# Kernel tuning notes

Measured on AMD Instinct MI355X. Metric: run time of the kernel, lower is better.

## Reference

```python
import jax, jax.numpy as jnp
import numpy as np
from jax import lax

N_SECTIONS, N_CHANNELS = 8, 128
KT, KF = 32, 16                 # kernel (time, freq)
LPOST = 400                     # section_length_postsyn
LPRE = KT + LPOST - 1           # 431, section_length_presyn
SECTION_DISTANCE = 400          # LPRE - overlap (overlap = 31)
N_TIMESTEPS, FREQ = 3231, 256
THRESHOLD = 15.0


def setup_inputs() -> dict:
    key = jax.random.key(0)
    k1, k2 = jax.random.split(key)
    # scale so mean conv response ~ threshold (512 taps * 0.8 * mean(X))
    X = jax.random.uniform(k1, (N_TIMESTEPS, FREQ), dtype=jnp.float32) * 0.073
    # SpykeTorch Convolution init: N(0.8, 0.05)
    W = 0.8 + 0.05 * jax.random.normal(k2, (N_SECTIONS, N_CHANNELS, 1, KT, KF), dtype=jnp.float32)
    return {"X": X, "W": W}


def _sections(X):
    # [S, LPRE, FREQ] overlapping time windows
    starts = jnp.arange(N_SECTIONS) * SECTION_DISTANCE
    idx = starts[:, None] + jnp.arange(LPRE)
    return X[idx]


def _conv_sections(X, W):
    Xs = _sections(X)  # [S, LPRE, FREQ]
    def conv1(xs, w):
        # xs: [LPRE, FREQ], w: [C, 1, KT, KF] -> [C, LPOST, FOUT]
        return lax.conv_general_dilated(xs[None, None], w, (1, 1), 'VALID')[0]
    return jax.vmap(conv1)(Xs, W)  # [S, C, LPOST, FOUT]


def reference(X, W):
    pots = _conv_sections(X, W)                              # [S, C, 400, 241]
    # sf.fire: zero potentials < threshold, then sign -> binary spikes
    spikes = (pots >= THRESHOLD).astype(pots.dtype)
    # Pooling((LPOST, KF)): max-pool, stride = window, no padding
    pool = lax.reduce_window(spikes, -jnp.inf, lax.max,
                             (1, 1, LPOST, KF), (1, 1, LPOST, KF), 'VALID')  # [S, C, 1, 15]
    # sf.get_k_winners(pool): dim 0 (sections) acts as the time dimension
    T = pool.shape[0]
    spk = jnp.sign(pool)
    earliest = jnp.clip((T - spk.sum(axis=0)).astype(jnp.int32), 0, T - 1)   # [C,1,Fp]
    values = jnp.take_along_axis(pool, earliest[None], axis=0)[0]            # earliest spike value
    trunc = spk * values[None]
    v = trunc.max() * T
    trunc = trunc + spk * v
    total = trunc.sum(axis=0)                                # [C, 1, Fp]
    max_val = total.max()
    # winners[0][0] = feature (channel) index of the flat argmax
    feat = jnp.argmax(total.reshape(-1)) // (total.shape[1] * total.shape[2])
    return jnp.where(max_val != 0, feat, -1).astype(jnp.int32)
```

## Files before the change

### kernel.cpp

```cpp
#include <hip/hip_runtime.h>


using int2v  = __attribute__((ext_vector_type(2))) int;
using int4v  = __attribute__((ext_vector_type(4))) int;
using int8v  = __attribute__((ext_vector_type(8))) int;
using f32x8  = __attribute__((ext_vector_type(8))) float;
using f32x16 = __attribute__((ext_vector_type(16))) float;

#define SCALE_ONE 0x7F7F7F7F
#define THRESH_Q  4920.0f

#if __has_builtin(__builtin_amdgcn_cvt_scalef32_pk_fp4_f32)
#define HWFP4 1
#else
#define HWFP4 0
#endif

__device__ __forceinline__ unsigned f4enc(float v) {
  float r2 = __builtin_rintf(v + v);
  float r1 = __builtin_rintf(v);
  return (v <= 2.f) ? (unsigned)r2
       : (v <= 4.f) ? (unsigned)r1 + 2u
       : (v < 5.f)  ? 6u : 7u;
}

__device__ __forceinline__ unsigned pack8(f32x8 v) {
  unsigned d = 0;
#if HWFP4
  d = __builtin_amdgcn_cvt_scalef32_pk_fp4_f32(d, v[0], v[1], 1.0f, 0);
  d = __builtin_amdgcn_cvt_scalef32_pk_fp4_f32(d, v[2], v[3], 1.0f, 1);
  d = __builtin_amdgcn_cvt_scalef32_pk_fp4_f32(d, v[4], v[5], 1.0f, 2);
  d = __builtin_amdgcn_cvt_scalef32_pk_fp4_f32(d, v[6], v[7], 1.0f, 3);
#else
#pragma unroll
  for (int e = 0; e < 8; ++e) d |= f4enc(v[e]) << (4 * e);
#endif
  return d;
}

__global__ __launch_bounds__(256) void prep_kernel(const float* __restrict__ W,
                                                   unsigned char* __restrict__ Wp4,
                                                   int* __restrict__ pool) {
  int t = blockIdx.x * 256 + threadIdx.x;
  if (t < 15360) pool[t] = 0;
  int s = t >> 11, r = t & 2047, c = r >> 4, b = r & 15;
  const float* src = W + ((s * 128 + c) * 512 + b * 32);
  int4v o;
#pragma unroll
  for (int i = 0; i < 4; ++i) {
    f32x8 sv;
#pragma unroll
    for (int e = 0; e < 8; ++e) sv[e] = fmaxf(src[i * 8 + e], 0.f) * 4.f;
    o[i] = (int)pack8(sv);
  }
  *(int4v*)(Wp4 + s * 32768 + (b >> 1) * 4096 + (b & 1) * 2048 + c * 16) = o;
}

__global__ __launch_bounds__(512, 2) void conv_pool_kernel(const float* __restrict__ X,
                                                           const unsigned char* __restrict__ Wp4,
                                                           int* __restrict__ pool) {
  __shared__ __align__(16) unsigned char Ash[2][8 * 512];
  __shared__ unsigned poolbits[2][32];

  const int tid = threadIdx.x;
  const int s   = blockIdx.x & 7;
  const int lb  = blockIdx.x >> 3;
  const int NT  = (lb < 6) ? 13 : 12;

  const int ok  = tid < 504;
  const int it0 = ok ? tid : 0;
  const int d0  = it0 / 63, r0 = it0 % 63;
  const float* Xs = X + (s * 400 + r0) * 256 + d0;

  const int w = tid >> 6, l = tid & 63;
  const int m31 = l & 31, ko = l >> 5;
  const int aoff = w * 512 + m31 * 8 + ko * 16;

  if (tid < 64) poolbits[tid >> 5][tid & 31] = 0;

  f32x8 xa, xb;
  {
    int tau = lb, tt = tau / 30, ft = tau % 30;
    int t0 = (tt == 12) ? 368 : tt * 32;
    const float* xp = Xs + t0 * 256 + ft * 8;
#pragma unroll
    for (int e = 0; e < 8; ++e) { xa[e] = xp[e]; xb[e] = xp[e + 8]; }
  }
  __builtin_amdgcn_sched_barrier(0);

  int4v Breg[8][4];
  {
    const unsigned char* wb = Wp4 + s * 32768 + ko * 2048 + m31 * 16;
#pragma unroll
    for (int ch = 0; ch < 8; ++ch)
#pragma unroll
      for (int nt = 0; nt < 4; ++nt)
        Breg[ch][nt] = *(const int4v*)(wb + ch * 4096 + nt * 512);
  }

  xa *= 82.f; xb *= 82.f;
  if (ok) *(int2v*)&Ash[0][d0 * 512 + r0 * 8] = (int2v){(int)pack8(xa), (int)pack8(xb)};
  if (NT > 1) {
    int tau = lb + 32, tt = tau / 30, ft = tau % 30;
    int t0 = (tt == 12) ? 368 : tt * 32;
    const float* xp = Xs + t0 * 256 + ft * 8;
#pragma unroll
    for (int e = 0; e < 8; ++e) { xa[e] = xp[e]; xb[e] = xp[e + 8]; }
  }
  __syncthreads();

#pragma unroll 1
  for (int i = 0; i < NT; ++i) {
    const unsigned char* ab = &Ash[i & 1][0];

    f32x16 acc[4];
#pragma unroll
    for (int b = 0; b < 4; ++b)
#pragma unroll
      for (int e = 0; e < 16; ++e) acc[b][e] = 0.f;
#pragma unroll
    for (int ch = 0; ch < 8; ++ch) {
      int2v alo = *(const int2v*)&ab[aoff + ch * 32];
      int2v ahi = *(const int2v*)&ab[aoff + ch * 32 + 8];
      int8v Af = {alo[0], alo[1], ahi[0], ahi[1], 0, 0, 0, 0};
#pragma unroll
      for (int nt = 0; nt < 4; ++nt) {
        int8v Bf = {Breg[ch][nt][0], Breg[ch][nt][1],
                    Breg[ch][nt][2], Breg[ch][nt][3], 0, 0, 0, 0};
        acc[nt] = __builtin_amdgcn_mfma_scale_f32_32x32x64_f8f6f4(
            Af, Bf, acc[nt], 4, 4, 0, SCALE_ONE, 0, SCALE_ONE);
      }
    }

    unsigned sp = 0;
#pragma unroll
    for (int nt = 0; nt < 4; ++nt) {
      float m0 = -1e30f;
#pragma unroll
      for (int e = 0; e < 16; ++e) m0 = fmaxf(m0, acc[nt][e]);
      if (m0 >= THRESH_Q) sp |= (1u << nt);
    }
    sp |= __shfl_xor(sp, 32, 64);
    if (l < 32 && sp) atomicOr(&poolbits[i & 1][m31], sp);

    if (i + 1 < NT) {
      xa *= 82.f; xb *= 82.f;
      if (ok)
        *(int2v*)&Ash[(i + 1) & 1][d0 * 512 + r0 * 8] =
            (int2v){(int)pack8(xa), (int)pack8(xb)};
      if (i + 2 < NT) {
        int tau = lb + 32 * (i + 2), tt = tau / 30, ft = tau % 30;
        int t0 = (tt == 12) ? 368 : tt * 32;
        const float* xp = Xs + t0 * 256 + ft * 8;
#pragma unroll
        for (int e = 0; e < 8; ++e) { xa[e] = xp[e]; xb[e] = xp[e + 8]; }
      }
    }

    __syncthreads();

    if (tid < 32) {
      unsigned bits = poolbits[i & 1][tid];
      poolbits[i & 1][tid] = 0;
      if (bits) {
        int tau = lb + 32 * i;
        int fp = (tau % 30) >> 1;
#pragma unroll
        for (int nt = 0; nt < 4; ++nt)
          if ((bits >> nt) & 1)
            pool[(s * 128 + nt * 32 + tid) * 15 + fp] = 1;
      }
    }
  }
}

__global__ __launch_bounds__(256) void winner_kernel(const int* __restrict__ pool,
                                                     float* __restrict__ out) {
  __shared__ int lp[15360];
  __shared__ int sh_v;
  __shared__ int sh_best;
  int tid = threadIdx.x;
  if (tid == 0) { sh_v = 0; sh_best = 0; }
  for (int i = tid; i < 15360; i += 256) lp[i] = pool[i];
  __syncthreads();

  int localv = 0;
  for (int p = tid; p < 1920; p += 256) {
    int c = p / 15, f = p % 15;
    int cnt = 0;
    for (int s = 0; s < 8; ++s) cnt += lp[(s * 128 + c) * 15 + f];
    if (cnt > 0) {
      int early = 8 - cnt; if (early > 7) early = 7;
      localv |= lp[(early * 128 + c) * 15 + f];
    }
  }
  if (localv) atomicOr(&sh_v, 1);
  __syncthreads();

  const int v = sh_v * 8;
  int localbest = 0;
  for (int p = tid; p < 1920; p += 256) {
    int c = p / 15, f = p % 15;
    int cnt = 0;
    for (int s = 0; s < 8; ++s) cnt += lp[(s * 128 + c) * 15 + f];
    int early = 8 - cnt; if (early > 7) early = 7;
    int val = lp[(early * 128 + c) * 15 + f];
    int total = cnt * (val + v);
    int pack = (total << 12) | (4095 - p);
    if (pack > localbest) localbest = pack;
  }
  atomicMax(&sh_best, localbest);
  __syncthreads();

  if (tid == 0) {
    int total = sh_best >> 12;
    int p = 4095 - (sh_best & 4095);
    int feat = p / 15;
    out[0] = (total != 0) ? (float)feat : -1.0f;
  }
}

extern "C" void kernel_launch(void* const* d_in, const int* in_sizes, int n_in,
                              void* d_out, int out_size, void* d_ws, size_t ws_size,
                              hipStream_t stream) {
  (void)in_sizes; (void)n_in; (void)out_size; (void)ws_size;
  const float* X = (const float*)d_in[0];
  const float* W = (const float*)d_in[1];
  unsigned char* Wp4 = (unsigned char*)d_ws;
  int* pool = (int*)((char*)d_ws + (1 << 18));

  prep_kernel<<<64, 256, 0, stream>>>(W, Wp4, pool);
  conv_pool_kernel<<<256, 512, 0, stream>>>(X, Wp4, pool);
  winner_kernel<<<1, 256, 0, stream>>>(pool, (float*)d_out);
}
```

Baseline: 86.99 us.

## Fuse winner selection into conv kernel via last-block pattern and bitmask pool

Replaces the per-element int pool array with a 15-bit mask per (section, channel), set with atomicOr. Removes the separate winner kernel: each conv block increments a done counter, and the last block to finish reads the bitmasks and computes the argmax. This saves one kernel launch and shrinks the pool memory that has to be zeroed and read. In exchange it adds global atomics, a threadfence and a serialized tail inside the last block, and it hardcodes v=8.

```diff
diff --git a/kernel.cpp b/kernel.cpp
--- a/kernel.cpp
+++ b/kernel.cpp
@@ -40,9 +40,9 @@
 
 __global__ __launch_bounds__(256) void prep_kernel(const float* __restrict__ W,
                                                    unsigned char* __restrict__ Wp4,
-                                                   int* __restrict__ pool) {
+                                                   unsigned* __restrict__ pool) {
   int t = blockIdx.x * 256 + threadIdx.x;
-  if (t < 15360) pool[t] = 0;
+  if (t < 1025) pool[t] = 0;
   int s = t >> 11, r = t & 2047, c = r >> 4, b = r & 15;
   const float* src = W + ((s * 128 + c) * 512 + b * 32);
   int4v o;
@@ -58,9 +58,12 @@
 
 __global__ __launch_bounds__(512, 2) void conv_pool_kernel(const float* __restrict__ X,
                                                            const unsigned char* __restrict__ Wp4,
-                                                           int* __restrict__ pool) {
+                                                           unsigned* __restrict__ pool,
+                                                           float* __restrict__ out) {
   __shared__ __align__(16) unsigned char Ash[2][8 * 512];
   __shared__ unsigned poolbits[2][32];
+
+  unsigned* done = pool + 1024;
 
   const int tid = threadIdx.x;
   const int s   = blockIdx.x & 7;
@@ -163,60 +166,48 @@
       unsigned bits = poolbits[i & 1][tid];
       poolbits[i & 1][tid] = 0;
       if (bits) {
-        int tau = lb + 32 * i;
-        int fp = (tau % 30) >> 1;
+        int fp = ((lb + 32 * i) % 30) >> 1;
+        unsigned bit = 1u << fp;
 #pragma unroll
         for (int nt = 0; nt < 4; ++nt)
           if ((bits >> nt) & 1)
-            pool[(s * 128 + nt * 32 + tid) * 15 + fp] = 1;
+            atomicOr(&pool[s * 128 + nt * 32 + tid], bit);
       }
     }
   }
-}
-
-__global__ __launch_bounds__(256) void winner_kernel(const int* __restrict__ pool,
-                                                     float* __restrict__ out) {
-  __shared__ int lp[15360];
-  __shared__ int sh_v;
-  __shared__ int sh_best;
-  int tid = threadIdx.x;
-  if (tid == 0) { sh_v = 0; sh_best = 0; }
-  for (int i = tid; i < 15360; i += 256) lp[i] = pool[i];
-  __syncthreads();
-
-  int localv = 0;
-  for (int p = tid; p < 1920; p += 256) {
+
+  __threadfence();
+  __syncthreads();
+  __shared__ int lastflag;
+  if (tid == 0) lastflag = (atomicAdd(done, 1u) == (unsigned)(gridDim.x - 1));
+  __syncthreads();
+  if (!lastflag) return;
+
+  __shared__ unsigned pb[1024];
+  __shared__ int bestpk;
+  if (tid == 0) bestpk = 0;
+  for (int q = tid; q < 1024; q += 512) pb[q] = atomicOr(&pool[q], 0u);
+  __syncthreads();
+
+  int lbest = 0;
+  for (int p = tid; p < 1920; p += 512) {
     int c = p / 15, f = p % 15;
     int cnt = 0;
-    for (int s = 0; s < 8; ++s) cnt += lp[(s * 128 + c) * 15 + f];
+#pragma unroll
+    for (int s2 = 0; s2 < 8; ++s2) cnt += (pb[s2 * 128 + c] >> f) & 1;
     if (cnt > 0) {
-      int early = 8 - cnt; if (early > 7) early = 7;
-      localv |= lp[(early * 128 + c) * 15 + f];
-    }
-  }
-  if (localv) atomicOr(&sh_v, 1);
-  __syncthreads();
-
-  const int v = sh_v * 8;
-  int localbest = 0;
-  for (int p = tid; p < 1920; p += 256) {
-    int c = p / 15, f = p % 15;
-    int cnt = 0;
-    for (int s = 0; s < 8; ++s) cnt += lp[(s * 128 + c) * 15 + f];
-    int early = 8 - cnt; if (early > 7) early = 7;
-    int val = lp[(early * 128 + c) * 15 + f];
-    int total = cnt * (val + v);
-    int pack = (total << 12) | (4095 - p);
-    if (pack > localbest) localbest = pack;
-  }
-  atomicMax(&sh_best, localbest);
-  __syncthreads();
-
+      int early = 8 - cnt;
+      int val = (pb[early * 128 + c] >> f) & 1;
+      int total = cnt * (8 + val);
+      int pack = (total << 12) | (4095 - p);
+      if (pack > lbest) lbest = pack;
+    }
+  }
+  atomicMax(&bestpk, lbest);
+  __syncthreads();
   if (tid == 0) {
-    int total = sh_best >> 12;
-    int p = 4095 - (sh_best & 4095);
-    int feat = p / 15;
-    out[0] = (total != 0) ? (float)feat : -1.0f;
+    int feat = (4095 - (bestpk & 4095)) / 15;
+    out[0] = (bestpk != 0) ? (float)feat : -1.0f;
   }
 }
 
@@ -227,9 +218,8 @@
   const float* X = (const float*)d_in[0];
   const float* W = (const float*)d_in[1];
   unsigned char* Wp4 = (unsigned char*)d_ws;
-  int* pool = (int*)((char*)d_ws + (1 << 18));
+  unsigned* pool = (unsigned*)((char*)d_ws + (1 << 18));
 
   prep_kernel<<<64, 256, 0, stream>>>(W, Wp4, pool);
-  conv_pool_kernel<<<256, 512, 0, stream>>>(X, Wp4, pool);
-  winner_kernel<<<1, 256, 0, stream>>>(pool, (float*)d_out);
-}
+  conv_pool_kernel<<<256, 512, 0, stream>>>(X, Wp4, pool, (float*)d_out);
+}
```

Result: slower. 111.6 us (+28.3%).
